# Kernel optimization log

Hardware: AMD Instinct MI355X
Metric: run time of the kernel (lower is better)

Reference implementation:

```python
import jax, jax.numpy as jnp
import numpy as np

NOISE_EPS = 1e-2   # Shazeer noisy-gating stddev floor
LN_EPS = 1e-6
LOSS_COEF = 0.01
K = 2              # num_activated_experts


def _layer_norm(x, w, b):
    mu = jnp.mean(x, axis=-1, keepdims=True)
    var = jnp.var(x, axis=-1, keepdims=True)
    return (x - mu) * jax.lax.rsqrt(var + LN_EPS) * w + b


def _cv_squared(v):
    return jnp.var(v) / (jnp.mean(v) ** 2 + 1e-10)


def _normal_cdf(z):
    return 0.5 * (1.0 + jax.scipy.special.erf(z / jnp.sqrt(jnp.asarray(2.0, z.dtype))))


def setup_inputs() -> dict:
    key = jax.random.key(0)
    ks = jax.random.split(key, 8)
    N, D, H, O, E = 8192, 512, 1024, 512, 8
    x = jax.random.normal(ks[0], (N, D), jnp.float32)
    x_offsets = jnp.sort(jax.random.randint(ks[1], (17,), 0, N)).astype(jnp.int64)
    noise = jax.random.normal(ks[2], (N, E), jnp.float32)
    s = 0.02
    return {
        "x": x,
        "x_offsets": x_offsets,
        "max_seq_len": 2048,
        "noise": noise,
        "norm_w": jnp.ones((D,), jnp.float32),
        "norm_bias": jnp.zeros((D,), jnp.float32),
        "w_gate": jax.random.normal(ks[3], (D, E), jnp.float32) * s,
        "w_noise": jax.random.normal(ks[4], (D, E), jnp.float32) * s,
        "W1": jax.random.normal(ks[5], (E, H, D), jnp.float32) * s,  # [E, model_d, input]
        "b1": jnp.zeros((E, H), jnp.float32),
        "W2": jax.random.normal(ks[6], (E, O, H), jnp.float32) * s,  # [E, output, model_d]
        "b2": jnp.zeros((E, O), jnp.float32),
        "output_weight": jax.random.normal(ks[7], (D, O), jnp.float32) * s,
    }


def reference(x, x_offsets, max_seq_len, noise, norm_w, norm_bias, w_gate, w_noise,
              W1, b1, W2, b2, output_weight):
    N, D = x.shape
    E = w_gate.shape[1]
    k_plus = min(K + 1, E)

    # pre-norm
    x_norm = _layer_norm(x, norm_w, norm_bias)

    # noisy top-k gating (training path)
    clean_logits = x_norm @ w_gate                      # [N, E]
    noise_stddev = jax.nn.softplus(x_norm @ w_noise) + NOISE_EPS
    noisy_logits = clean_logits + noise * noise_stddev

    top_logits, top_indices = jax.lax.top_k(noisy_logits, k_plus)   # [N, k+1]
    top_k_logits = top_logits[:, :K]
    top_k_indices = top_indices[:, :K]
    top_k_gates = jax.nn.softmax(top_k_logits, axis=-1)             # [N, K]

    rows = jnp.arange(N)[:, None]
    gates = jnp.zeros((N, E), top_k_gates.dtype).at[rows, top_k_indices].set(top_k_gates)

    # load = prob each expert is in top-k under the gating noise (Shazeer)
    flat = top_logits.reshape(-1)
    pos_in = jnp.arange(N) * k_plus + K
    thr_in = flat[pos_in][:, None]          # (k+1)-th value: threshold if already in
    thr_out = flat[pos_in - 1][:, None]     # k-th value: threshold if currently out
    is_in = noisy_logits > thr_in
    prob_in = _normal_cdf((clean_logits - thr_in) / noise_stddev)
    prob_out = _normal_cdf((clean_logits - thr_out) / noise_stddev)
    load_probs = jnp.where(is_in, prob_in, prob_out)                # [N, E]

    loss = LOSS_COEF * (_cv_squared(gates.sum(0)) + _cv_squared(load_probs.sum(0)))

    # dispatch stats: tokens per expert
    lengths = jnp.zeros((E,), jnp.float32).at[top_k_indices.reshape(-1)].add(1.0)
    load = lengths / lengths.sum()

    # grouped expert MLP (dense one-hot combine; gates are 0 for unrouted experts)
    h = jnp.einsum('nd,ehd->neh', x_norm, W1) + b1                  # [N, E, H]
    a = jax.nn.silu(h)
    y_e = jnp.einsum('neh,eoh->neo', a, W2) + b2                    # [N, E, O]
    y_moe = jnp.einsum('ne,neo->no', gates, y_e)                    # [N, O]

    # shared expert: addmm(y, shared_x=x, output_weight)
    y = y_moe + x @ output_weight
    return y, loss, load
```

## Files before the change

kernel.cpp:

```cpp
#include <hip/hip_runtime.h>
#include <math.h>

typedef unsigned short u16;
typedef unsigned int u32;

#define N_ROWS 8192
#define DDIM 512
#define HDIM 1024
#define ODIM 512
#define NEXP 8
#define MAXPAIRS (N_ROWS * 2)
#define MAXPOS (MAXPAIRS + NEXP * 128)
#define MAXTILES (MAXPOS / 128)

#define SM_CNT 0
#define SM_CUR 8
#define SM_AOFF 16
#define SM_WORDS 64

using short8 = __attribute__((ext_vector_type(8))) short;
using float4v = __attribute__((ext_vector_type(4))) float;

__device__ __forceinline__ u16 f2bf(float f) {
    union { float f; u32 u; } v; v.f = f;
    u32 u = v.u;
    return (u16)((u + 0x7fffu + ((u >> 16) & 1u)) >> 16);
}

__device__ __forceinline__ void async_copy16(u16* lds, const u16* g) {
    __builtin_amdgcn_global_load_lds(
        (const __attribute__((address_space(1))) void*)g,
        (__attribute__((address_space(3))) void*)lds, 16, 0, 0);
}

#define MEGA_GATE 512
#define MEGA_W1 2048
#define MEGA_OWT 256
#define MEGA_BUCKET 68
#define MEGA_W2 2048
#define MEGA_BLOCKS (MEGA_GATE + MEGA_W1 + MEGA_OWT + MEGA_BUCKET + MEGA_W2)
__global__ __launch_bounds__(256) void mega_kernel(
    const float* __restrict__ x, const float* __restrict__ noise,
    const float* __restrict__ norm_w, const float* __restrict__ norm_b,
    const float* __restrict__ w_gate, const float* __restrict__ w_noise,
    const float* __restrict__ W1, const float* __restrict__ ow,
    const float* __restrict__ W2,
    u16* __restrict__ xnorm_bf, u16* __restrict__ x_bf,
    int* __restrict__ pair_expert, float* __restrict__ pair_gate,
    u16* __restrict__ W1b, u16* __restrict__ owT, u16* __restrict__ W2b,
    int* __restrict__ bucket_rows, int* __restrict__ small, float* __restrict__ zeropage,
    float* __restrict__ partial_g, float* __restrict__ partial_l, int* __restrict__ partial_c)
{
    __shared__ __align__(16) float sh[32 * 33 + 8];
    int b = blockIdx.x, tid = threadIdx.x;

    if (b >= MEGA_GATE) {
        int cb = b - MEGA_GATE;
        if (cb < MEGA_W1) {
            size_t i = (size_t)cb * 512 + tid;
#pragma unroll
            for (int t = 0; t < 2; t++, i += 256) {
                float4 v = ((const float4*)W1)[i];
                ushort4 o;
                o.x = f2bf(v.x); o.y = f2bf(v.y); o.z = f2bf(v.z); o.w = f2bf(v.w);
                ((ushort4*)W1b)[i] = o;
            }
        } else if (cb < MEGA_W1 + MEGA_OWT) {
            float (*tile)[33] = (float(*)[33])sh;
            int t = cb - MEGA_W1;
            int bx = (t & 15) * 32, by = (t >> 4) * 32;
            int tx = tid & 31, ty = tid >> 5;
            for (int r = ty; r < 32; r += 8) tile[r][tx] = ow[(size_t)(by + r) * ODIM + bx + tx];
            __syncthreads();
            for (int r = ty; r < 32; r += 8) owT[(size_t)(bx + r) * DDIM + by + tx] = f2bf(tile[tx][r]);
        } else if (cb < MEGA_W1 + MEGA_OWT + MEGA_BUCKET) {
            int lb = cb - MEGA_W1 - MEGA_OWT;
            int i = lb * 256 + tid;
            if (i < MAXPOS) bucket_rows[i] = -1;
            if (lb == 0) {
                if (tid < SM_WORDS) small[tid] = 0;
                zeropage[tid] = 0.f; zeropage[tid + 256] = 0.f;
            }
        } else {
            int j = cb - MEGA_W1 - MEGA_OWT - MEGA_BUCKET;
            size_t i = (size_t)j * 512 + tid;
#pragma unroll
            for (int t = 0; t < 2; t++, i += 256) {
                float4 v = ((const float4*)W2)[i];
                ushort4 o;
                o.x = f2bf(v.x); o.y = f2bf(v.y); o.z = f2bf(v.z); o.w = f2bf(v.w);
                ((ushort4*)W2b)[i] = o;
            }
        }
        return;
    }

    float* lg = sh;
    float* blk_g = sh + 16 * 17;
    float* blk_l = blk_g + 8;
    int* blk_c = (int*)(blk_l + 8);

    int wave = tid >> 6, lane = tid & 63;
    if (tid < 8) { blk_g[tid] = 0.f; blk_l[tid] = 0.f; blk_c[tid] = 0; }
    float nw[8], nb[8];
#pragma unroll
    for (int j = 0; j < 8; j++) { nw[j] = norm_w[j * 64 + lane]; nb[j] = norm_b[j * 64 + lane]; }

    bool l5 = (lane & 32) != 0, l4 = (lane & 16) != 0;
    bool l3 = (lane & 8) != 0, l2 = (lane & 4) != 0;

    for (int half = 0; half < 2; ++half) {
        float xv[2][8], mu[2], rstd[2];
#pragma unroll
        for (int r = 0; r < 2; ++r) {
            int row = b * 16 + wave * 4 + half * 2 + r;
            const float* xr = x + (size_t)row * DDIM;
            float s = 0.f, s2 = 0.f;
#pragma unroll
            for (int j = 0; j < 8; j++) { float v = xr[j * 64 + lane]; xv[r][j] = v; s += v; s2 += v * v; }
#pragma unroll
            for (int o = 32; o; o >>= 1) { s += __shfl_xor(s, o, 64); s2 += __shfl_xor(s2, o, 64); }
            mu[r] = s * (1.f / DDIM);
            float var = s2 * (1.f / DDIM) - mu[r] * mu[r];
            rstd[r] = rsqrtf(var + 1e-6f);
        }
        float acc[2][16];
#pragma unroll
        for (int r = 0; r < 2; ++r)
#pragma unroll
            for (int e = 0; e < 16; e++) acc[r][e] = 0.f;
#pragma unroll
        for (int j = 0; j < 8; j++) {
            int d = j * 64 + lane;
            float4 wg0 = *(const float4*)&w_gate[d * 8];
            float4 wg1 = *(const float4*)&w_gate[d * 8 + 4];
            float4 wn0 = *(const float4*)&w_noise[d * 8];
            float4 wn1 = *(const float4*)&w_noise[d * 8 + 4];
#pragma unroll
            for (int r = 0; r < 2; ++r) {
                int row = b * 16 + wave * 4 + half * 2 + r;
                float v = (xv[r][j] - mu[r]) * rstd[r] * nw[j] + nb[j];
                xnorm_bf[(size_t)row * DDIM + d] = f2bf(v);
                x_bf[(size_t)row * DDIM + d] = f2bf(xv[r][j]);
                acc[r][0] += v * wg0.x; acc[r][1] += v * wg0.y;
                acc[r][2] += v * wg0.z; acc[r][3] += v * wg0.w;
                acc[r][4] += v * wg1.x; acc[r][5] += v * wg1.y;
                acc[r][6] += v * wg1.z; acc[r][7] += v * wg1.w;
                acc[r][8] += v * wn0.x; acc[r][9] += v * wn0.y;
                acc[r][10] += v * wn0.z; acc[r][11] += v * wn0.w;
                acc[r][12] += v * wn1.x; acc[r][13] += v * wn1.y;
                acc[r][14] += v * wn1.z; acc[r][15] += v * wn1.w;
            }
        }
#pragma unroll
        for (int r = 0; r < 2; ++r) {
            int lrow16 = wave * 4 + half * 2 + r;
            float t8[8];
#pragma unroll
            for (int v = 0; v < 8; v++) {
                float snd = l5 ? acc[r][v] : acc[r][v + 8];
                float kp = l5 ? acc[r][v + 8] : acc[r][v];
                t8[v] = kp + __shfl_xor(snd, 32, 64);
            }
            float t4[4];
#pragma unroll
            for (int v = 0; v < 4; v++) {
                float snd = l4 ? t8[v] : t8[v + 4];
                float kp = l4 ? t8[v + 4] : t8[v];
                t4[v] = kp + __shfl_xor(snd, 16, 64);
            }
            float t2[2];
#pragma unroll
            for (int v = 0; v < 2; v++) {
                float snd = l3 ? t4[v] : t4[v + 2];
                float kp = l3 ? t4[v + 2] : t4[v];
                t2[v] = kp + __shfl_xor(snd, 8, 64);
            }
            float snd = l2 ? t2[0] : t2[1];
            float kp = l2 ? t2[1] : t2[0];
            float t1 = kp + __shfl_xor(snd, 4, 64);
            t1 += __shfl_xor(t1, 2, 64);
            t1 += __shfl_xor(t1, 1, 64);
            if ((lane & 3) == 0) lg[lrow16 * 17 + ((lane >> 2) & 15)] = t1;
        }
    }
    __syncthreads();

    if (tid < 16) {
        int row = b * 16 + tid;
        float cl[8], sd[8], nz[8];
#pragma unroll
        for (int e = 0; e < 8; e++) {
            cl[e] = lg[tid * 17 + e];
            float t = lg[tid * 17 + 8 + e];
            float sp = fmaxf(t, 0.f) + log1pf(expf(-fabsf(t)));
            sd[e] = sp + 0.01f;
            nz[e] = cl[e] + noise[(size_t)row * NEXP + e] * sd[e];
        }
        int idx[3]; float val[3]; u32 msk = 0;
#pragma unroll
        for (int t = 0; t < 3; t++) {
            float best = -INFINITY; int bi = 0;
#pragma unroll
            for (int e = 0; e < 8; e++)
                if (!((msk >> e) & 1) && nz[e] > best) { best = nz[e]; bi = e; }
            idx[t] = bi; val[t] = best; msk |= 1u << bi;
        }
        float e1 = expf(val[1] - val[0]);
        float g0 = 1.f / (1.f + e1), g1 = e1 / (1.f + e1);
        float thr_in = val[2], thr_out = val[1];

        pair_expert[row * 2] = idx[0]; pair_gate[row * 2] = g0;
        pair_expert[row * 2 + 1] = idx[1]; pair_gate[row * 2 + 1] = g1;
        atomicAdd(&blk_g[idx[0]], g0); atomicAdd(&blk_g[idx[1]], g1);
        atomicAdd(&blk_c[idx[0]], 1); atomicAdd(&blk_c[idx[1]], 1);
#pragma unroll
        for (int e = 0; e < 8; e++) {
            float thr = (nz[e] > thr_in) ? thr_in : thr_out;
            float z = (cl[e] - thr) / sd[e];
            float p = 0.5f * (1.f + erff(z * 0.70710678118654752f));
            atomicAdd(&blk_l[e], p);
        }
    }
    __syncthreads();
    if (tid < 8) {
        partial_g[b * 8 + tid] = blk_g[tid];
        partial_l[b * 8 + tid] = blk_l[tid];
        partial_c[b * 8 + tid] = blk_c[tid];
    }
}

__global__ __launch_bounds__(256) void scatter_kernel(
    const int* __restrict__ pair_expert, const float* __restrict__ pair_gate,
    const float* __restrict__ partial_g, const float* __restrict__ partial_l,
    const int* __restrict__ partial_c,
    int* __restrict__ small, int* __restrict__ bucket_rows, float* __restrict__ gate_by_pos,
    int* __restrict__ rowpos,
    float* __restrict__ out_loss, float* __restrict__ out_load)
{
    __shared__ int aoff[NEXP + 1];
    __shared__ int blk_cnt[NEXP];
    __shared__ int blk_base[NEXP];
    __shared__ int ired[256];
    __shared__ float fred[256];
    __shared__ float gsum[NEXP], lsum[NEXP];
    int tid = threadIdx.x;
    int e = tid & 7, g = tid >> 3;

    int s = 0;
    for (int k = g; k < MEGA_GATE; k += 32) s += partial_c[k * 8 + e];
    ired[tid] = s;
    if (tid < NEXP) blk_cnt[tid] = 0;
    __syncthreads();
    if (tid < 64) ired[tid] = ired[tid] + ired[tid + 64] + ired[tid + 128] + ired[tid + 192];
    __syncthreads();
    if (tid < 8) {
        int t = 0;
        for (int q = tid; q < 64; q += 8) t += ired[q];
        ired[tid] = t;
    }
    __syncthreads();
    if (tid == 0) {
        int acc = 0; aoff[0] = 0;
        for (int k = 0; k < NEXP; k++) { acc += (ired[k] + 127) & ~127; aoff[k + 1] = acc; }
    }
    __syncthreads();

    int p = blockIdx.x * 256 + tid;
    int pe = pair_expert[p];
    int local = atomicAdd(&blk_cnt[pe], 1);
    __syncthreads();
    if (tid < NEXP)
        blk_base[tid] = aoff[tid] + atomicAdd(&small[SM_CUR + tid], blk_cnt[tid]);
    if (blockIdx.x == 0 && tid < NEXP + 1) small[SM_AOFF + tid] = aoff[tid];
    __syncthreads();
    int pos = blk_base[pe] + local;
    bucket_rows[pos] = p >> 1;
    gate_by_pos[pos] = pair_gate[p];
    rowpos[p] = pos;

    if (blockIdx.x == 0) {
        float sg = 0.f, sl = 0.f;
        for (int k = g; k < MEGA_GATE; k += 32) { sg += partial_g[k * 8 + e]; sl += partial_l[k * 8 + e]; }
        fred[tid] = sg;
        __syncthreads();
        if (tid < 64) fred[tid] = fred[tid] + fred[tid + 64] + fred[tid + 128] + fred[tid + 192];
        __syncthreads();
        if (tid < 8) { float t = 0.f; for (int q = tid; q < 64; q += 8) t += fred[q]; gsum[tid] = t; }
        __syncthreads();
        fred[tid] = sl;
        __syncthreads();
        if (tid < 64) fred[tid] = fred[tid] + fred[tid + 64] + fred[tid + 128] + fred[tid + 192];
        __syncthreads();
        if (tid < 8) { float t = 0.f; for (int q = tid; q < 64; q += 8) t += fred[q]; lsum[tid] = t; }
        __syncthreads();
        if (tid == 0) {
            float cv[2];
            for (int t = 0; t < 2; t++) {
                const float* v = t ? lsum : gsum;
                float m = 0.f;
                for (int k = 0; k < NEXP; k++) m += v[k];
                m *= (1.f / NEXP);
                float var = 0.f;
                for (int k = 0; k < NEXP; k++) { float d = v[k] - m; var += d * d; }
                var *= (1.f / NEXP);
                cv[t] = var / (m * m + 1e-10f);
            }
            out_loss[0] = 0.01f * (cv[0] + cv[1]);
            int tot = 0;
            for (int k = 0; k < NEXP; k++) tot += ired[k];
            float inv = 1.f / (float)tot;
            for (int k = 0; k < NEXP; k++) out_load[k] = (float)ired[k] * inv;
        }
    }
}

__global__ __launch_bounds__(512) void gemmA_kernel(
    const u16* __restrict__ xnorm, const u16* __restrict__ W1b,
    const u16* __restrict__ xbf, const u16* __restrict__ owT,
    const int* __restrict__ bucket_rows, const int* __restrict__ small,
    const float* __restrict__ b1, const u16* __restrict__ zeropage,
    u16* __restrict__ a_buf, float* __restrict__ y)
{
    constexpr int KD = 512;
    __shared__ __align__(16) u16 As[2][128 * 32];
    __shared__ __align__(16) u16 Bs[2][256 * 32];

    int tid = threadIdx.x;
    int wave = tid >> 6, lane = tid & 63;
    const int lrow = lane >> 2;
    const int kcol = (((lane & 3) ^ ((lane >> 3) & 3)) * 8);
    int wm = (wave >> 2) * 64, wn = (wave & 3) * 64;
    int fr = lane & 15, kq = lane >> 4;
    const int kg = ((kq ^ ((fr >> 1) & 3)) * 8);

    bool m0 = blockIdx.y < 4;
    int base, bn, e = 0;
    const u16 *ga0, *gb0, *gb1;
    if (m0) {
        base = blockIdx.x * 128;
        if (base >= small[SM_AOFF + 8]) return;
        while (e < 7 && base >= small[SM_AOFF + e + 1]) ++e;
        bn = blockIdx.y * 256;
        int r0 = bucket_rows[base + wave * 16 + lrow];
        ga0 = ((r0 < 0) ? zeropage : xnorm + (size_t)r0 * KD) + kcol;
        const u16* Bsel = W1b + (size_t)e * HDIM * KD;
        gb0 = Bsel + (size_t)(bn + wave * 32 + lrow) * KD + kcol;
        gb1 = Bsel + (size_t)(bn + wave * 32 + 16 + lrow) * KD + kcol;
    } else {
        int j = blockIdx.x;
        if (j >= 128) return;
        base = (j >> 1) * 128;
        bn = (j & 1) * 256;
        ga0 = xbf + (size_t)(base + wave * 16 + lrow) * KD + kcol;
        gb0 = owT + (size_t)(bn + wave * 32 + lrow) * KD + kcol;
        gb1 = owT + (size_t)(bn + wave * 32 + 16 + lrow) * KD + kcol;
    }
    const int ofA = (wave * 16) * 32;
    const int ofB0 = (wave * 32) * 32;
    const int ofB1 = (wave * 32 + 16) * 32;

    float4v acc[4][4];
#pragma unroll
    for (int i = 0; i < 4; i++)
#pragma unroll
        for (int j = 0; j < 4; j++) acc[i][j] = (float4v){0.f, 0.f, 0.f, 0.f};

    constexpr int nk = KD >> 5;
    async_copy16(&As[0][ofA], ga0);
    async_copy16(&Bs[0][ofB0], gb0);
    async_copy16(&Bs[0][ofB1], gb1);
    __syncthreads();

    int cur = 0;
    for (int t = 0; t < nk; ++t) {
        int nxt = cur ^ 1;
        if (t + 1 < nk) {
            int k1 = (t + 1) << 5;
            async_copy16(&As[nxt][ofA], ga0 + k1);
            async_copy16(&Bs[nxt][ofB0], gb0 + k1);
            async_copy16(&Bs[nxt][ofB1], gb1 + k1);
        }
        short8 af[4], bf[4];
#pragma unroll
        for (int mt = 0; mt < 4; mt++) af[mt] = *(const short8*)&As[cur][(wm + mt * 16 + fr) * 32 + kg];
#pragma unroll
        for (int nt = 0; nt < 4; nt++) bf[nt] = *(const short8*)&Bs[cur][(wn + nt * 16 + fr) * 32 + kg];
#pragma unroll
        for (int mt = 0; mt < 4; mt++)
#pragma unroll
            for (int nt = 0; nt < 4; nt++)
                acc[mt][nt] = __builtin_amdgcn_mfma_f32_16x16x32_bf16(af[mt], bf[nt], acc[mt][nt], 0, 0, 0);
        __syncthreads();
        cur = nxt;
    }

    int rbase = (lane >> 4) * 4, c16 = lane & 15;
    if (m0) {
#pragma unroll
        for (int nt = 0; nt < 4; nt++) {
            int gn = bn + wn + nt * 16 + c16;
            float bv = b1[e * HDIM + gn];
#pragma unroll
            for (int mt = 0; mt < 4; mt++) {
                int gm = base + wm + mt * 16 + rbase;
#pragma unroll
                for (int r = 0; r < 4; r++) {
                    float h = acc[mt][nt][r] + bv;
                    float a = h * __builtin_amdgcn_rcpf(1.f + __expf(-h));
                    a_buf[(size_t)(gm + r) * HDIM + gn] = f2bf(a);
                }
            }
        }
    } else {
#pragma unroll
        for (int mt = 0; mt < 4; mt++) {
            int gm = base + wm + mt * 16 + rbase;
#pragma unroll
            for (int nt = 0; nt < 4; nt++) {
                int gn = bn + wn + nt * 16 + c16;
#pragma unroll
                for (int r = 0; r < 4; r++)
                    y[(size_t)(gm + r) * ODIM + gn] = acc[mt][nt][r];
            }
        }
    }
}

__global__ __launch_bounds__(512) void gemmB_kernel(
    const u16* __restrict__ a_buf, const u16* __restrict__ W2b,
    const int* __restrict__ bucket_rows, const int* __restrict__ small,
    const float* __restrict__ b2, const float* __restrict__ gate_by_pos,
    float* __restrict__ ye)
{
    constexpr int KD = 1024;
    __shared__ __align__(16) u16 As[2][128 * 32];
    __shared__ __align__(16) u16 Bs[2][256 * 32];

    int tid = threadIdx.x;
    int wave = tid >> 6, lane = tid & 63;
    const int lrow = lane >> 2;
    const int kcol = (((lane & 3) ^ ((lane >> 3) & 3)) * 8);
    int wm = (wave >> 2) * 64, wn = (wave & 3) * 64;
    int fr = lane & 15, kq = lane >> 4;
    const int kg = ((kq ^ ((fr >> 1) & 3)) * 8);

    int base = blockIdx.x * 128;
    if (base >= small[SM_AOFF + 8]) return;
    int e = 0;
    while (e < 7 && base >= small[SM_AOFF + e + 1]) ++e;
    int bn = blockIdx.y * 256;

    const u16* ga0 = a_buf + (size_t)(base + wave * 16 + lrow) * KD + kcol;
    const u16* Bsel = W2b + (size_t)e * ODIM * KD;
    const u16* gb0 = Bsel + (size_t)(bn + wave * 32 + lrow) * KD + kcol;
    const u16* gb1 = Bsel + (size_t)(bn + wave * 32 + 16 + lrow) * KD + kcol;
    const int ofA = (wave * 16) * 32;
    const int ofB0 = (wave * 32) * 32;
    const int ofB1 = (wave * 32 + 16) * 32;

    float4v acc[4][4];
#pragma unroll
    for (int i = 0; i < 4; i++)
#pragma unroll
        for (int j = 0; j < 4; j++) acc[i][j] = (float4v){0.f, 0.f, 0.f, 0.f};

    constexpr int nk = KD >> 5;
    async_copy16(&As[0][ofA], ga0);
    async_copy16(&Bs[0][ofB0], gb0);
    async_copy16(&Bs[0][ofB1], gb1);
    __syncthreads();

    int cur = 0;
    for (int t = 0; t < nk; ++t) {
        int nxt = cur ^ 1;
        if (t + 1 < nk) {
            int k1 = (t + 1) << 5;
            async_copy16(&As[nxt][ofA], ga0 + k1);
            async_copy16(&Bs[nxt][ofB0], gb0 + k1);
            async_copy16(&Bs[nxt][ofB1], gb1 + k1);
        }
        short8 af[4], bf[4];
#pragma unroll
        for (int mt = 0; mt < 4; mt++) af[mt] = *(const short8*)&As[cur][(wm + mt * 16 + fr) * 32 + kg];
#pragma unroll
        for (int nt = 0; nt < 4; nt++) bf[nt] = *(const short8*)&Bs[cur][(wn + nt * 16 + fr) * 32 + kg];
#pragma unroll
        for (int mt = 0; mt < 4; mt++)
#pragma unroll
            for (int nt = 0; nt < 4; nt++)
                acc[mt][nt] = __builtin_amdgcn_mfma_f32_16x16x32_bf16(af[mt], bf[nt], acc[mt][nt], 0, 0, 0);
        __syncthreads();
        cur = nxt;
    }

    int rbase = (lane >> 4) * 4, c16 = lane & 15;
#pragma unroll
    for (int mt = 0; mt < 4; mt++) {
        int pos0 = base + wm + mt * 16 + rbase;
        int rows[4]; float gs[4];
#pragma unroll
        for (int r = 0; r < 4; r++) { rows[r] = bucket_rows[pos0 + r]; gs[r] = gate_by_pos[pos0 + r]; }
#pragma unroll
        for (int nt = 0; nt < 4; nt++) {
            int gn = bn + wn + nt * 16 + c16;
            float b2v = b2[e * ODIM + gn];
#pragma unroll
            for (int r = 0; r < 4; r++) {
                if (rows[r] >= 0)
                    ye[(size_t)(pos0 + r) * ODIM + gn] = gs[r] * (acc[mt][nt][r] + b2v);
            }
        }
    }
}

__global__ __launch_bounds__(256) void combine_kernel(
    const float* __restrict__ ye, const int* __restrict__ rowpos,
    float* __restrict__ y)
{
    int tid = threadIdx.x;
    int row = blockIdx.x * 16 + (tid >> 4);
    int c0 = (tid & 15) * 32;
    int p0 = rowpos[row * 2];
    int p1 = rowpos[row * 2 + 1];
    const float4* e0 = (const float4*)(ye + (size_t)p0 * ODIM + c0);
    const float4* e1 = (const float4*)(ye + (size_t)p1 * ODIM + c0);
    float4* yp = (float4*)(y + (size_t)row * ODIM + c0);
#pragma unroll
    for (int i = 0; i < 8; i++) {
        float4 a = yp[i], b = e0[i], c = e1[i];
        a.x += b.x + c.x; a.y += b.y + c.y; a.z += b.z + c.z; a.w += b.w + c.w;
        yp[i] = a;
    }
}

extern "C" void kernel_launch(void* const* d_in, const int* in_sizes, int n_in,
                              void* d_out, int out_size, void* d_ws, size_t ws_size,
                              hipStream_t stream)
{
    (void)in_sizes; (void)n_in; (void)out_size; (void)ws_size;
    const float* x = (const float*)d_in[0];
    const float* noise = (const float*)d_in[3];
    const float* norm_w = (const float*)d_in[4];
    const float* norm_b = (const float*)d_in[5];
    const float* w_gate = (const float*)d_in[6];
    const float* w_noise = (const float*)d_in[7];
    const float* W1 = (const float*)d_in[8];
    const float* b1 = (const float*)d_in[9];
    const float* W2 = (const float*)d_in[10];
    const float* b2 = (const float*)d_in[11];
    const float* ow = (const float*)d_in[12];

    float* y = (float*)d_out;
    float* out_loss = y + (size_t)N_ROWS * ODIM;
    float* out_load = out_loss + 1;

    char* ws = (char*)d_ws;
    size_t off = 0;
    auto alloc = [&](size_t b) { size_t p = off; off = (off + b + 255) & ~(size_t)255; return p; };
    u16* xnorm_bf = (u16*)(ws + alloc((size_t)N_ROWS * DDIM * 2));
    u16* x_bf     = (u16*)(ws + alloc((size_t)N_ROWS * DDIM * 2));
    u16* W1b      = (u16*)(ws + alloc((size_t)NEXP * HDIM * DDIM * 2));
    u16* W2b      = (u16*)(ws + alloc((size_t)NEXP * ODIM * HDIM * 2));
    u16* owT      = (u16*)(ws + alloc((size_t)DDIM * ODIM * 2));
    u16* a_buf    = (u16*)(ws + alloc((size_t)MAXPOS * HDIM * 2));
    float* ye     = (float*)(ws + alloc((size_t)MAXPOS * ODIM * 4));
    int* pair_expert = (int*)(ws + alloc((size_t)MAXPAIRS * 4));
    float* pair_gate = (float*)(ws + alloc((size_t)MAXPAIRS * 4));
    float* gate_by_pos = (float*)(ws + alloc((size_t)MAXPOS * 4));
    int* bucket_rows = (int*)(ws + alloc((size_t)MAXPOS * 4));
    int* rowpos      = (int*)(ws + alloc((size_t)MAXPAIRS * 4));
    int* small       = (int*)(ws + alloc(SM_WORDS * 4));
    float* zeropage  = (float*)(ws + alloc(2048));
    float* partial_g = (float*)(ws + alloc((size_t)MEGA_GATE * NEXP * 4));
    float* partial_l = (float*)(ws + alloc((size_t)MEGA_GATE * NEXP * 4));
    int* partial_c   = (int*)(ws + alloc((size_t)MEGA_GATE * NEXP * 4));

    mega_kernel<<<MEGA_BLOCKS, 256, 0, stream>>>(
        x, noise, norm_w, norm_b, w_gate, w_noise, W1, ow, W2,
        xnorm_bf, x_bf, pair_expert, pair_gate, W1b, owT, W2b,
        bucket_rows, small, zeropage, partial_g, partial_l, partial_c);
    scatter_kernel<<<MAXPAIRS / 256, 256, 0, stream>>>(pair_expert, pair_gate,
                                                       partial_g, partial_l, partial_c,
                                                       small, bucket_rows, gate_by_pos, rowpos,
                                                       out_loss, out_load);
    gemmA_kernel<<<dim3(MAXTILES, 5), 512, 0, stream>>>(xnorm_bf, W1b,
                                                        x_bf, owT, bucket_rows, small, b1,
                                                        (const u16*)zeropage, a_buf, y);
    gemmB_kernel<<<dim3(MAXTILES, 2), 512, 0, stream>>>(a_buf, W2b, bucket_rows,
                                                        small, b2, gate_by_pos, ye);
    combine_kernel<<<N_ROWS / 16, 256, 0, stream>>>(ye, rowpos, y);
}
```

Before: 234.5 us.

## Triple-buffer LDS tiles in expert GEMMs with fine-grained vmcnt waits

Both expert GEMM kernels move from a double-buffered LDS pipeline to a triple-buffered one that prefetches two k-steps ahead. The per-iteration full __syncthreads pair becomes one explicit s_waitcnt vmcnt(3) followed by a single s_barrier, so loads for tile t+2 stay in flight while tile t is consumed. The aim is to hide global-memory latency and remove one barrier per iteration. The cost is 1.5x the LDS footprint (72KB per block), which may cut occupancy. Correctness also depends on the async copies being tracked by vmcnt and on the LDS read from the previous iteration finishing before the buffer is overwritten.

```diff
diff --git a/kernel.cpp b/kernel.cpp
--- a/kernel.cpp
+++ b/kernel.cpp
@@ -323,8 +323,8 @@
     u16* __restrict__ a_buf, float* __restrict__ y)
 {
     constexpr int KD = 512;
-    __shared__ __align__(16) u16 As[2][128 * 32];
-    __shared__ __align__(16) u16 Bs[2][256 * 32];
+    __shared__ __align__(16) u16 As[3][128 * 32];
+    __shared__ __align__(16) u16 Bs[3][256 * 32];
 
     int tid = threadIdx.x;
     int wave = tid >> 6, lane = tid & 63;
@@ -370,16 +370,22 @@
     async_copy16(&As[0][ofA], ga0);
     async_copy16(&Bs[0][ofB0], gb0);
     async_copy16(&Bs[0][ofB1], gb1);
-    __syncthreads();
+    async_copy16(&As[1][ofA], ga0 + 32);
+    async_copy16(&Bs[1][ofB0], gb0 + 32);
+    async_copy16(&Bs[1][ofB1], gb1 + 32);
 
     int cur = 0;
     for (int t = 0; t < nk; ++t) {
-        int nxt = cur ^ 1;
-        if (t + 1 < nk) {
-            int k1 = (t + 1) << 5;
-            async_copy16(&As[nxt][ofA], ga0 + k1);
-            async_copy16(&Bs[nxt][ofB0], gb0 + k1);
-            async_copy16(&Bs[nxt][ofB1], gb1 + k1);
+        if (t == nk - 1) asm volatile("s_waitcnt vmcnt(0)" ::: "memory");
+        else             asm volatile("s_waitcnt vmcnt(3)" ::: "memory");
+        __builtin_amdgcn_s_barrier();
+        __builtin_amdgcn_sched_barrier(0);
+        if (t + 2 < nk) {
+            int nb = cur + 2; if (nb >= 3) nb -= 3;
+            int k2 = (t + 2) << 5;
+            async_copy16(&As[nb][ofA], ga0 + k2);
+            async_copy16(&Bs[nb][ofB0], gb0 + k2);
+            async_copy16(&Bs[nb][ofB1], gb1 + k2);
         }
         short8 af[4], bf[4];
 #pragma unroll
@@ -391,8 +397,7 @@
 #pragma unroll
             for (int nt = 0; nt < 4; nt++)
                 acc[mt][nt] = __builtin_amdgcn_mfma_f32_16x16x32_bf16(af[mt], bf[nt], acc[mt][nt], 0, 0, 0);
-        __syncthreads();
-        cur = nxt;
+        cur = cur + 1; if (cur >= 3) cur = 0;
     }
 
     int rbase = (lane >> 4) * 4, c16 = lane & 15;
@@ -434,8 +439,8 @@
     float* __restrict__ ye)
 {
     constexpr int KD = 1024;
-    __shared__ __align__(16) u16 As[2][128 * 32];
-    __shared__ __align__(16) u16 Bs[2][256 * 32];
+    __shared__ __align__(16) u16 As[3][128 * 32];
+    __shared__ __align__(16) u16 Bs[3][256 * 32];
 
     int tid = threadIdx.x;
     int wave = tid >> 6, lane = tid & 63;
@@ -469,16 +474,22 @@
     async_copy16(&As[0][ofA], ga0);
     async_copy16(&Bs[0][ofB0], gb0);
     async_copy16(&Bs[0][ofB1], gb1);
-    __syncthreads();
+    async_copy16(&As[1][ofA], ga0 + 32);
+    async_copy16(&Bs[1][ofB0], gb0 + 32);
+    async_copy16(&Bs[1][ofB1], gb1 + 32);
 
     int cur = 0;
     for (int t = 0; t < nk; ++t) {
-        int nxt = cur ^ 1;
-        if (t + 1 < nk) {
-            int k1 = (t + 1) << 5;
-            async_copy16(&As[nxt][ofA], ga0 + k1);
-            async_copy16(&Bs[nxt][ofB0], gb0 + k1);
-            async_copy16(&Bs[nxt][ofB1], gb1 + k1);
+        if (t == nk - 1) asm volatile("s_waitcnt vmcnt(0)" ::: "memory");
+        else             asm volatile("s_waitcnt vmcnt(3)" ::: "memory");
+        __builtin_amdgcn_s_barrier();
+        __builtin_amdgcn_sched_barrier(0);
+        if (t + 2 < nk) {
+            int nb = cur + 2; if (nb >= 3) nb -= 3;
+            int k2 = (t + 2) << 5;
+            async_copy16(&As[nb][ofA], ga0 + k2);
+            async_copy16(&Bs[nb][ofB0], gb0 + k2);
+            async_copy16(&Bs[nb][ofB1], gb1 + k2);
         }
         short8 af[4], bf[4];
 #pragma unroll
@@ -490,8 +501,7 @@
 #pragma unroll
             for (int nt = 0; nt < 4; nt++)
                 acc[mt][nt] = __builtin_amdgcn_mfma_f32_16x16x32_bf16(af[mt], bf[nt], acc[mt][nt], 0, 0, 0);
-        __syncthreads();
-        cur = nxt;
+        cur = cur + 1; if (cur >= 3) cur = 0;
     }
 
     int rbase = (lane >> 4) * 4, c16 = lane & 15;
```

After: 260.0 us. 1.11x slower.
